# Kernel tuning notes

Hardware: AMD Instinct MI355X
Metric: run time of the kernel (lower is better)

## Reference

```python
import jax, jax.numpy as jnp
import numpy as np

K_SIZE = 5  # neighborhood window

def _extract_patches(x, k):
    # tf.image.extract_patches with stride 1, SAME (zero) padding.
    # x: [B,H,W,C] -> [B,H,W,k*k,C]
    pad = k // 2
    B, H, W, C = x.shape
    xp = jnp.pad(x, ((0, 0), (pad, pad), (pad, pad), (0, 0)))
    # fixed small k*k loop (25 shifted views), stacked along patch axis
    return jnp.stack([xp[:, i:i + H, j:j + W, :]
                      for i in range(k) for j in range(k)], axis=3)

def setup_inputs() -> dict:
    key = jax.random.key(0)
    k1, k2, k3 = jax.random.split(key, 3)
    B, H, W, C, BIN = 2, 256, 256, 32, 32
    return {
        "main": jax.random.normal(k1, (B, H, W, C), dtype=jnp.float32),
        "ref": jax.random.normal(k2, (B, H, W, C), dtype=jnp.float32),
        "ref_value": jax.random.normal(k3, (B, H, W, BIN), dtype=jnp.float32),
    }

def reference(main, ref, ref_value):
    # mode='dot': local-window dot-product attention
    ref_stacked = _extract_patches(ref, K_SIZE)          # [B,H,W,k*k,C]
    attn = jnp.einsum('bhwc,bhwkc->bhwk', main, ref_stacked)
    attn = jax.nn.softmax(attn, axis=-1)                 # [B,H,W,k*k]
    # aggregate_mode='weighted_sum'
    ref_value_stacked = _extract_patches(ref_value, K_SIZE)  # [B,H,W,k*k,bin]
    return jnp.einsum('bhwk,bhwki->bhwi', attn, ref_value_stacked)
```

## Files before the change

kernel.cpp:

```cpp
#include <hip/hip_runtime.h>


__global__ void __launch_bounds__(256)
local_attn_kernel(const float* __restrict__ main_p,
                  const float* __restrict__ ref_p,
                  const float* __restrict__ rv_p,
                  float* __restrict__ out_p)
{
    const int lane = threadIdx.x & 63;
    const int wv   = threadIdx.x >> 6;
    const int cg   = lane & 7;
    const int pw   = lane >> 3;

    const int b     = blockIdx.x;
    const int batch = b >> 10;
    const int tb    = b & 1023;
    const int ty    = tb >> 3;
    const int tx    = tb & 7;
    const int w0    = tx * 32 + wv * 8 + pw;
    const int h0    = ty * 2;
    const int bbase = batch << 16;

    const float4* m4 = (const float4*)main_p;
    const float4* r4 = (const float4*)ref_p;
    const float4* v4 = (const float4*)rv_p;
    float4*       o4 = (float4*)out_p;

    const float4 m0 = m4[(bbase + (h0 + 0) * 256 + w0) * 8 + cg];
    const float4 m1 = m4[(bbase + (h0 + 1) * 256 + w0) * 8 + cg];

    float  sum0 = 0.f, sum1 = 0.f;
    float4 a0 = make_float4(0.f, 0.f, 0.f, 0.f);
    float4 a1 = make_float4(0.f, 0.f, 0.f, 0.f);

#pragma unroll
    for (int ri = 0; ri < 6; ++ri) {
        const int   hh   = h0 + ri - 2;
        const float rok  = ((unsigned)hh < 256u) ? 1.0f : 0.0f;
        const int   rowb = bbase + min(max(hh, 0), 255) * 256;
#pragma unroll
        for (int dj = 0; dj < 5; ++dj) {
            const int   ww  = w0 + dj - 2;
            const float msk = rok * (((unsigned)ww < 256u) ? 1.0f : 0.0f);
            const int   a   = (rowb + min(max(ww, 0), 255)) * 8 + cg;

            const float4 r = r4[a];
            const float4 v = v4[a];

            if (ri < 5) {
                float s = m0.x * r.x + m0.y * r.y + m0.z * r.z + m0.w * r.w;
                s += __shfl_xor(s, 1, 64);
                s += __shfl_xor(s, 2, 64);
                s += __shfl_xor(s, 4, 64);
                const float e  = __expf(s * msk);
                const float wk = e * msk;
                sum0 += e;
                a0.x += wk * v.x; a0.y += wk * v.y;
                a0.z += wk * v.z; a0.w += wk * v.w;
            }
            if (ri >= 1) {
                float s = m1.x * r.x + m1.y * r.y + m1.z * r.z + m1.w * r.w;
                s += __shfl_xor(s, 1, 64);
                s += __shfl_xor(s, 2, 64);
                s += __shfl_xor(s, 4, 64);
                const float e  = __expf(s * msk);
                const float wk = e * msk;
                sum1 += e;
                a1.x += wk * v.x; a1.y += wk * v.y;
                a1.z += wk * v.z; a1.w += wk * v.w;
            }
        }
    }

    const float i0 = 1.0f / sum0;
    const float i1 = 1.0f / sum1;
    a0.x *= i0; a0.y *= i0; a0.z *= i0; a0.w *= i0;
    a1.x *= i1; a1.y *= i1; a1.z *= i1; a1.w *= i1;

    o4[(bbase + (h0 + 0) * 256 + w0) * 8 + cg] = a0;
    o4[(bbase + (h0 + 1) * 256 + w0) * 8 + cg] = a1;
}

extern "C" void kernel_launch(void* const* d_in, const int* in_sizes, int n_in,
                              void* d_out, int out_size, void* d_ws, size_t ws_size,
                              hipStream_t stream)
{
    const float* main_p = (const float*)d_in[0];
    const float* ref_p  = (const float*)d_in[1];
    const float* rv_p   = (const float*)d_in[2];
    float*       out_p  = (float*)d_out;

    const int npix   = in_sizes[0] / 32;
    const int blocks = npix / 64;
    local_attn_kernel<<<blocks, 256, 0, stream>>>(main_p, ref_p, rv_p, out_p);
}
```

Measured before the change: 106.1 us.

## Stage ref and ref_value halo tiles in shared memory before window loop

Each block now cooperatively loads a 6-row by 36-column halo tile of ref and ref_value into LDS, then reads the 5x5 neighborhoods from shared memory instead of issuing 30 global float4 loads per thread. The aim is to cut redundant global/L2 traffic from overlapping windows. In exchange it uses about 55 KB of LDS per block, which may limit occupancy, and adds a __syncthreads barrier.

```diff
diff --git a/kernel.cpp b/kernel.cpp
--- a/kernel.cpp
+++ b/kernel.cpp
@@ -1,5 +1,10 @@
 #include <hip/hip_runtime.h>
 
+
+#define LROWS 6
+#define LCOLS 36
+#define L4PERROW (LCOLS * 8)
+#define L4TOTAL  (LROWS * L4PERROW)
 
 __global__ void __launch_bounds__(256)
 local_attn_kernel(const float* __restrict__ main_p,
@@ -7,8 +12,12 @@
                   const float* __restrict__ rv_p,
                   float* __restrict__ out_p)
 {
-    const int lane = threadIdx.x & 63;
-    const int wv   = threadIdx.x >> 6;
+    __shared__ float4 s_r[L4TOTAL];
+    __shared__ float4 s_v[L4TOTAL];
+
+    const int tid  = threadIdx.x;
+    const int lane = tid & 63;
+    const int wv   = tid >> 6;
     const int cg   = lane & 7;
     const int pw   = lane >> 3;
 
@@ -17,17 +26,35 @@
     const int tb    = b & 1023;
     const int ty    = tb >> 3;
     const int tx    = tb & 7;
-    const int w0    = tx * 32 + wv * 8 + pw;
     const int h0    = ty * 2;
+    const int wt    = tx * 32;
     const int bbase = batch << 16;
+
+    const int src_c0 = min(max(wt - 2, 0), 256 - LCOLS);
 
     const float4* m4 = (const float4*)main_p;
     const float4* r4 = (const float4*)ref_p;
     const float4* v4 = (const float4*)rv_p;
     float4*       o4 = (float4*)out_p;
 
+#pragma unroll
+    for (int t = 0; t < 7; ++t) {
+        const int idx = tid + t * 256;
+        if (idx < L4TOTAL) {
+            const int row = idx / L4PERROW;
+            const int rem = idx - row * L4PERROW;
+            const int hh  = min(max(h0 + row - 2, 0), 255);
+            const int g   = (bbase + hh * 256 + src_c0) * 8 + rem;
+            s_r[idx] = r4[g];
+            s_v[idx] = v4[g];
+        }
+    }
+
+    const int w0 = wt + wv * 8 + pw;
     const float4 m0 = m4[(bbase + (h0 + 0) * 256 + w0) * 8 + cg];
     const float4 m1 = m4[(bbase + (h0 + 1) * 256 + w0) * 8 + cg];
+
+    __syncthreads();
 
     float  sum0 = 0.f, sum1 = 0.f;
     float4 a0 = make_float4(0.f, 0.f, 0.f, 0.f);
@@ -35,17 +62,17 @@
 
 #pragma unroll
     for (int ri = 0; ri < 6; ++ri) {
-        const int   hh   = h0 + ri - 2;
-        const float rok  = ((unsigned)hh < 256u) ? 1.0f : 0.0f;
-        const int   rowb = bbase + min(max(hh, 0), 255) * 256;
+        const int   hh  = h0 + ri - 2;
+        const float rok = ((unsigned)hh < 256u) ? 1.0f : 0.0f;
 #pragma unroll
         for (int dj = 0; dj < 5; ++dj) {
             const int   ww  = w0 + dj - 2;
             const float msk = rok * (((unsigned)ww < 256u) ? 1.0f : 0.0f);
-            const int   a   = (rowb + min(max(ww, 0), 255)) * 8 + cg;
+            const int   lc  = min(max(ww, 0), 255) - src_c0;
+            const int   li  = (ri * LCOLS + lc) * 8 + cg;
 
-            const float4 r = r4[a];
-            const float4 v = v4[a];
+            const float4 r = s_r[li];
+            const float4 v = s_v[li];
 
             if (ri < 5) {
                 float s = m0.x * r.x + m0.y * r.y + m0.z * r.z + m0.w * r.w;
```

Result: no change. 108.2 us (+2.0%).
